# Kernel optimization log

Measured on AMD Instinct MI355X. Metric: run time of the kernel, lower is better.

The kernel has to match this reference:

```python
import jax, jax.numpy as jnp
import numpy as np
import math

EMBED_DIM = 512
NUM_HEADS = 8
NUM_EXPERTS = 16
TOP_K = 8
B, T = 2, 1024


def setup_inputs() -> dict:
    key = jax.random.key(0)
    ks = jax.random.split(key, 16)
    d, E = EMBED_DIM, NUM_EXPERTS
    hdim = 4 * d  # expert hidden width
    s = 0.02
    inp = {
        "x": jax.random.normal(ks[0], (B, T, d), jnp.float32),
        # RMSNorm params (init ones, matching torch module)
        "g": jnp.ones((d,), jnp.float32),
        "b": jnp.ones((d,), jnp.float32),
        # attention
        "c_attn_w": jax.random.normal(ks[1], (d, 3 * d), jnp.float32) * s,
        "c_attn_b": jnp.zeros((3 * d,), jnp.float32),
        "alpha": jnp.ones((NUM_HEADS,), jnp.float32),
        "c_proj_w": jax.random.normal(ks[2], (d, d), jnp.float32) * s,
        "c_proj_b": jnp.zeros((d,), jnp.float32),
        # router
        "router_w": jax.random.normal(ks[3], (d, E), jnp.float32) * s,
        "router_b": jnp.zeros((E,), jnp.float32),
        # stacked expert params: Linear(d,4d) -> SwiGLU(4d,4d) -> Linear(4d,d)
        "w_in": jax.random.normal(ks[4], (E, d, hdim), jnp.float32) * s,
        "b_in": jnp.zeros((E, hdim), jnp.float32),
        "w1": jax.random.normal(ks[5], (E, hdim, 2 * hdim), jnp.float32) * s,
        "b1": jnp.zeros((E, 2 * hdim), jnp.float32),
        "w2": jax.random.normal(ks[6], (E, hdim, hdim), jnp.float32) * s,
        "b2": jnp.zeros((E, hdim), jnp.float32),
        "w_out": jax.random.normal(ks[7], (E, hdim, d), jnp.float32) * s,
        "b_out": jnp.zeros((E, d), jnp.float32),
    }
    return inp


def _block(x, g, b, c_attn_w, c_attn_b, alpha, c_proj_w, c_proj_b,
           router_w, router_b, w_in, b_in, w1, b1, w2, b2, w_out, b_out):
    Bb, Tt, C = x.shape
    H = alpha.shape[0]
    hd = C // H
    E = router_b.shape[0]

    # RMSNorm (note: additive b, per original module)
    rms = jnp.sqrt(jnp.mean(x * x, axis=-1, keepdims=True) + 1e-6)
    xn = (x / rms) * g + b

    # QK-normalized causal attention
    qkv = xn @ c_attn_w + c_attn_b                      # [B,T,3C]
    q, k, v = jnp.split(qkv, 3, axis=-1)
    def heads(t):
        return t.reshape(Bb, Tt, H, hd).transpose(0, 2, 1, 3)  # [B,H,T,hd]
    q, k, v = heads(q), heads(k), heads(v)
    eps = 1e-5
    q_hat = q / (jnp.linalg.norm(q, axis=-1, keepdims=True) + eps)
    k_hat = k / (jnp.linalg.norm(k, axis=-1, keepdims=True) + eps)
    factor = (alpha * math.sqrt(hd)).reshape(1, H, 1, 1)
    q_scaled = q_hat * factor
    # SDPA default scale = 1/sqrt(head_dim)
    scores = jnp.einsum("bhqd,bhkd->bhqk", q_scaled, k_hat) / math.sqrt(hd)
    causal = jnp.tril(jnp.ones((Tt, Tt), bool))
    scores = jnp.where(causal, scores, -jnp.inf)
    att = jax.nn.softmax(scores, axis=-1)
    y = jnp.einsum("bhqk,bhkd->bhqd", att, v)
    y = y.transpose(0, 2, 1, 3).reshape(Bb, Tt, C)
    y = y @ c_proj_w + c_proj_b
    x = x + y

    # Router + top-8 normalized gates
    routes = jax.nn.softmax(x @ router_w + router_b, axis=-1)  # [B,T,E]
    probs, idx = jax.lax.top_k(routes, TOP_K)
    probs = probs / jnp.sum(probs, axis=-1, keepdims=True)
    # combine weights per expert: [B,T,E]
    gates = jnp.sum(jax.nn.one_hot(idx, E, dtype=x.dtype) * probs[..., None], axis=2)

    # Dense expert evaluation (faithful math: unselected tokens get zero gate)
    N = Bb * Tt
    xf = x.reshape(N, C)
    gf = gates.reshape(N, E)
    h = jnp.einsum("nd,edf->enf", xf, w_in) + b_in[:, None, :]      # [E,N,4d]
    c = jnp.einsum("enf,efg->eng", h, w1) + b1[:, None, :]          # [E,N,8d]
    a, bb2 = jnp.split(c, 2, axis=-1)
    s = (bb2 * jax.nn.sigmoid(bb2)) * a                              # SwiGLU
    o = jnp.einsum("enf,efg->eng", s, w2) + b2[:, None, :]          # [E,N,4d]
    eo = jnp.einsum("enf,efd->end", o, w_out) + b_out[:, None, :]   # [E,N,d]
    moe = jnp.einsum("end,ne->nd", eo, gf).reshape(Bb, Tt, C)
    return x + moe


def reference(x, g, b, c_attn_w, c_attn_b, alpha, c_proj_w, c_proj_b,
              router_w, router_b, w_in, b_in, w1, b1, w2, b2, w_out, b_out):
    return _block(x, g, b, c_attn_w, c_attn_b, alpha, c_proj_w, c_proj_b,
                  router_w, router_b, w_in, b_in, w1, b1, w2, b2, w_out, b_out)
```

## Files before the change

kernel.cpp:

```cpp
#include <hip/hip_runtime.h>
#include <stdint.h>

#define DEVI __device__ __forceinline__
#define FENCE() asm volatile("" ::: "memory")
#define BAR() do{ FENCE(); __builtin_amdgcn_s_barrier(); FENCE(); }while(0)

typedef short short8 __attribute__((ext_vector_type(8)));
typedef short short4v __attribute__((ext_vector_type(4)));
typedef float f32x4 __attribute__((ext_vector_type(4)));

DEVI float bf2f(unsigned short s){ union{unsigned u; float f;} x; x.u = ((unsigned)s)<<16; return x.f; }
DEVI unsigned short f2bf(float f){ union{float f; unsigned u;} x; x.f=f; unsigned r = x.u + 0x7fff + ((x.u>>16)&1); return (unsigned short)(r>>16); }

DEVI void gload_lds16(const void* g, void* l){
  __builtin_amdgcn_global_load_lds((const __attribute__((address_space(1))) unsigned int*)g,
                                   (__attribute__((address_space(3))) unsigned int*)l, 16, 0, 0);
}

__global__ __launch_bounds__(256)
void transpose_cvt(const float* __restrict__ in, unsigned short* __restrict__ out, int K, int N)
{
  __shared__ float tile[32][33];
  size_t zoff = (size_t)blockIdx.z * K * N;
  const float* src = in + zoff;
  unsigned short* dst = out + zoff;
  int kb = blockIdx.y*32, nb = blockIdx.x*32;
  int t = threadIdx.x;
  int tr = t>>3, tc = (t&7)*4;
  float4 v = *(const float4*)(src + (size_t)(kb+tr)*N + nb + tc);
  tile[tr][tc+0]=v.x; tile[tr][tc+1]=v.y; tile[tr][tc+2]=v.z; tile[tr][tc+3]=v.w;
  __syncthreads();
  short4v ov;
  ov[0] = (short)f2bf(tile[tc+0][tr]);
  ov[1] = (short)f2bf(tile[tc+1][tr]);
  ov[2] = (short)f2bf(tile[tc+2][tr]);
  ov[3] = (short)f2bf(tile[tc+3][tr]);
  *(short4v*)(dst + (size_t)(nb+tr)*K + kb + tc) = ov;
}

__global__ __launch_bounds__(256)
void rmsnorm_k(const float* __restrict__ x, const float* __restrict__ gw,
               const float* __restrict__ bw, unsigned short* __restrict__ xn)
{
  int row = blockIdx.x*4 + (threadIdx.x>>6);
  int lane = threadIdx.x & 63;
  const float* xr = x + (size_t)row*512 + lane*8;
  float4 a = *(const float4*)xr;
  float4 c = *(const float4*)(xr+4);
  float ss = a.x*a.x+a.y*a.y+a.z*a.z+a.w*a.w + c.x*c.x+c.y*c.y+c.z*c.z+c.w*c.w;
  #pragma unroll
  for (int m=1;m<64;m<<=1) ss += __shfl_xor(ss, m);
  float inv = 1.0f / sqrtf(ss*(1.f/512.f) + 1e-6f);
  const float* gr = gw + lane*8; const float* br = bw + lane*8;
  float4 g0=*(const float4*)gr, g1=*(const float4*)(gr+4);
  float4 b0=*(const float4*)br, b1=*(const float4*)(br+4);
  short8 o;
  o[0]=(short)f2bf(a.x*inv*g0.x + b0.x);
  o[1]=(short)f2bf(a.y*inv*g0.y + b0.y);
  o[2]=(short)f2bf(a.z*inv*g0.z + b0.z);
  o[3]=(short)f2bf(a.w*inv*g0.w + b0.w);
  o[4]=(short)f2bf(c.x*inv*g1.x + b1.x);
  o[5]=(short)f2bf(c.y*inv*g1.y + b1.y);
  o[6]=(short)f2bf(c.z*inv*g1.z + b1.z);
  o[7]=(short)f2bf(c.w*inv*g1.w + b1.w);
  *(short8*)(xn + (size_t)row*512 + lane*8) = o;
}

#define MFMA_QUAD(MQ) do{ \
  __builtin_amdgcn_s_setprio(1); \
  _Pragma("unroll") \
  for (int m=(MQ)*2; m<(MQ)*2+2; m++){ \
    _Pragma("unroll") \
    for (int n=0;n<4;n++){ \
      _Pragma("unroll") \
      for (int kk=0;kk<2;kk++) \
        acc[m][n] = __builtin_amdgcn_mfma_f32_16x16x32_bf16(afr[m][kk], bfr[n][kk], acc[m][n], 0,0,0); \
    } \
  } \
  __builtin_amdgcn_s_setprio(0); \
}while(0)

template<int EPI>
__global__ __launch_bounds__(512, 2)
void gemm8(const unsigned short* __restrict__ A, const unsigned short* __restrict__ B,
           const float* __restrict__ bias,
           float* __restrict__ Cf, unsigned short* __restrict__ Ch,
           const unsigned short* __restrict__ aux,
           int M, int N, int K,
           const int* __restrict__ off, long long strideBz, long long strideBiasz)
{
  __shared__ char smem[131072];
  int z = blockIdx.z;
  int rowbase = 0, Mz = M;
  if (off){ rowbase = off[z]; Mz = off[z+1] - rowbase; }
  int row0 = blockIdx.y * 256;
  if (row0 >= Mz) return;
  int col0 = blockIdx.x * 256;
  const unsigned short* Ab = A + (size_t)(rowbase + row0) * K;
  const unsigned short* Bb = B + (size_t)z * strideBz + (size_t)col0 * K;
  const float* biasz = bias + (size_t)z * strideBiasz;

  int tid = threadIdx.x;
  int lane = tid & 63, w = tid >> 6;
  int lrow = lane & 15, lg = lane >> 4;
  int wm = w >> 2, wn = w & 3;

  f32x4 acc[8][4];
  #pragma unroll
  for (int i=0;i<8;i++){
    #pragma unroll
    for (int j=0;j<4;j++) acc[i][j] = f32x4{0.f,0.f,0.f,0.f};
  }

  int nkt = K >> 6;

  auto stage = [&](int kt2, int H){
    if (kt2 >= nkt) return;
    char* sl = smem + (size_t)(kt2 & 1) * 65536 + (size_t)H * 16384;
    int k0 = kt2 << 6;
    const unsigned short* src = (H < 2) ? Ab : Bb;
    int rbase = (H & 1) * 128;
    #pragma unroll
    for (int i=0;i<2;i++){
      int si = i*512 + tid;
      int r = si >> 3, kb = (si & 7) ^ (r & 7);
      gload_lds16(src + (size_t)(rbase + r)*K + k0 + kb*8, sl + si*16);
    }
  };

  stage(0,0); stage(0,1); stage(0,2); stage(0,3);
  stage(1,0); stage(1,1); stage(1,2);
  asm volatile("s_waitcnt vmcnt(6)" ::: "memory");
  BAR();

  for (int kt = 0; kt < nkt; kt++){
    char* sl = smem + (size_t)(kt & 1) * 65536;
    char* sB = sl + 32768;
    short8 afr[8][2], bfr[4][2];
    #pragma unroll
    for (int n=0;n<4;n++){
      int ct = wn*64 + n*16 + lrow;
      #pragma unroll
      for (int kk=0;kk<2;kk++)
        bfr[n][kk] = *(const short8*)(sB + ct*128 + (((lg + kk*4) ^ (ct&7))<<4));
    }
    #pragma unroll
    for (int m=0;m<8;m++){
      int rt = wm*128 + m*16 + lrow;
      #pragma unroll
      for (int kk=0;kk<2;kk++)
        afr[m][kk] = *(const short8*)(sl + rt*128 + (((lg + kk*4) ^ (rt&7))<<4));
    }
    stage(kt+1, 3);
    BAR();
    asm volatile("s_waitcnt lgkmcnt(0)" ::: "memory");
    __builtin_amdgcn_sched_barrier(0);
    MFMA_QUAD(0);
    BAR();
    stage(kt+2, 0);
    BAR();
    MFMA_QUAD(1);
    BAR();
    stage(kt+2, 1);
    BAR();
    MFMA_QUAD(2);
    BAR();
    stage(kt+2, 2);
    if (kt + 2 < nkt) { asm volatile("s_waitcnt vmcnt(6)" ::: "memory"); }
    else              { asm volatile("s_waitcnt vmcnt(0)" ::: "memory"); }
    BAR();
    MFMA_QUAD(3);
    BAR();
  }

  #pragma unroll
  for (int m=0;m<8;m++){
    int rloc = wm*128 + m*16 + lg*4;
    #pragma unroll
    for (int j=0;j<4;j++){
      int row = row0 + rloc + j;
      if (row < Mz){
        size_t rg = (size_t)(rowbase + row);
        #pragma unroll
        for (int n=0;n<4;n++){
          int col = col0 + wn*64 + n*16 + lrow;
          float v = acc[m][n][j] + biasz[col];
          size_t idx = rg * N + col;
          if constexpr (EPI == 0){
            Cf[idx] = v;
          } else if constexpr (EPI == 1){
            Ch[idx] = f2bf(v);
          } else {
            float a = bf2f(aux[idx]);
            float sg = v / (1.f + __expf(-v));
            Ch[idx] = f2bf(a * sg);
          }
        }
      }
    }
  }
}

__global__ __launch_bounds__(256)
void gemm_proj(const unsigned short* __restrict__ A, const unsigned short* __restrict__ B,
               const float* __restrict__ bias,
               float* __restrict__ Cf, unsigned short* __restrict__ Ch,
               const float* __restrict__ resid, int M, int N, int K)
{
  __shared__ char smem[32768];
  char* smA = smem; char* smB = smem + 16384;
  int row0 = blockIdx.y * 128;
  int col0 = blockIdx.x * 128;
  int t = threadIdx.x, w = t>>6, lane = t&63;
  int lrow = lane&15, lg = lane>>4;
  int wr = w>>1, wc = w&1;

  f32x4 acc[4][4];
  #pragma unroll
  for (int i=0;i<4;i++){
    #pragma unroll
    for (int j=0;j<4;j++) acc[i][j] = f32x4{0.f,0.f,0.f,0.f};
  }
  const size_t Abase = (size_t)row0 * K;
  const size_t Bbase = (size_t)col0 * K;
  int nkt = K >> 6;
  for (int kt=0; kt<nkt; kt++){
    __syncthreads();
    int k0 = kt*64;
    #pragma unroll
    for (int i=0;i<4;i++){
      int s = (i*4 + w)*64 + lane;
      int r = s>>3;
      int kb = (s&7) ^ (r&7);
      gload_lds16(A + Abase + (size_t)r*K + k0 + kb*8, smA + (size_t)(i*4+w)*1024);
      gload_lds16(B + Bbase + (size_t)r*K + k0 + kb*8, smB + (size_t)(i*4+w)*1024);
    }
    __syncthreads();
    #pragma unroll
    for (int ks=0; ks<2; ks++){
      short8 af[4], bf[4];
      int kbb = lg + ks*4;
      #pragma unroll
      for (int m=0;m<4;m++){
        int rt = wr*64 + m*16 + lrow;
        af[m] = *(const short8*)(smA + rt*128 + ((kbb ^ (rt&7))<<4));
      }
      #pragma unroll
      for (int n=0;n<4;n++){
        int rt = wc*64 + n*16 + lrow;
        bf[n] = *(const short8*)(smB + rt*128 + ((kbb ^ (rt&7))<<4));
      }
      #pragma unroll
      for (int m=0;m<4;m++){
        #pragma unroll
        for (int n=0;n<4;n++)
          acc[m][n] = __builtin_amdgcn_mfma_f32_16x16x32_bf16(af[m], bf[n], acc[m][n], 0,0,0);
      }
    }
  }
  #pragma unroll
  for (int m=0;m<4;m++){
    int rloc = wr*64 + m*16 + lg*4;
    #pragma unroll
    for (int j=0;j<4;j++){
      int row = row0 + rloc + j;
      size_t rg = (size_t)row;
      #pragma unroll
      for (int n=0;n<4;n++){
        int col = col0 + wc*64 + n*16 + lrow;
        float v = acc[m][n][j] + bias[col];
        size_t idx = rg * N + col;
        v += resid[idx];
        Cf[idx] = v;
        Ch[idx] = f2bf(v);
      }
    }
  }
}

__global__ __launch_bounds__(256)
void prep_qkv(const float* __restrict__ qkv, const float* __restrict__ alpha,
              unsigned short* __restrict__ q_s, unsigned short* __restrict__ k_hat,
              unsigned short* __restrict__ v_t)
{
  int idx = blockIdx.x*4 + (threadIdx.x>>6);
  int lane = threadIdx.x & 63;
  int h = idx & 7, bt = idx >> 3;
  size_t base = (size_t)bt*1536 + h*64 + lane;
  float qv = qkv[base], kv = qkv[base+512], vv = qkv[base+1024];
  float qs2 = qv*qv, ks2 = kv*kv;
  #pragma unroll
  for (int m=1;m<64;m<<=1){ qs2 += __shfl_xor(qs2, m); ks2 += __shfl_xor(ks2, m); }
  float qh = qv / (sqrtf(qs2) + 1e-5f) * alpha[h];
  float kh = kv / (sqrtf(ks2) + 1e-5f);
  int b = bt >> 10, tt = bt & 1023;
  size_t hb = ((size_t)(b*8+h))*1024*64;
  q_s[hb + (size_t)tt*64 + lane] = f2bf(qh);
  k_hat[hb + (size_t)tt*64 + lane] = f2bf(kh);
  v_t[((size_t)(b*8+h)*64 + lane)*1024 + tt] = f2bf(vv);
}

__global__ __launch_bounds__(256)
void attn_k(const unsigned short* __restrict__ q_s, const unsigned short* __restrict__ k_hat,
            const unsigned short* __restrict__ v_t, unsigned short* __restrict__ y)
{
  __shared__ char sm[51200];
  char* smK = sm + 18432;
  char* smV = sm + 34816;
  int qt = blockIdx.x, bh = blockIdx.y;
  int b = bh>>3, h = bh&7;
  int t = threadIdx.x, w = t>>6, lane = t&63;
  int lrow = lane&15, lg = lane>>4;
  int q0 = qt*128;
  const size_t hQK = (size_t)bh*1024*64;
  const size_t hV  = (size_t)bh*64*1024;

  #pragma unroll
  for (int i=0;i<4;i++){
    int s = (i*4+w)*64 + lane;
    int r = s>>3, kb = (s&7)^(r&7);
    gload_lds16(q_s + hQK + (size_t)(q0+r)*64 + kb*8, sm + (size_t)(i*4+w)*1024);
  }
  __syncthreads();
  short8 qf[2][2];
  #pragma unroll
  for (int mf=0;mf<2;mf++){
    #pragma unroll
    for (int ks=0;ks<2;ks++){
      int rt = w*32 + mf*16 + lrow;
      int kbb = lg + ks*4;
      qf[mf][ks] = *(const short8*)(sm + rt*128 + ((kbb^(rt&7))<<4));
    }
  }
  f32x4 oacc[2][4];
  #pragma unroll
  for (int i=0;i<2;i++){
    #pragma unroll
    for (int j=0;j<4;j++) oacc[i][j] = f32x4{0.f,0.f,0.f,0.f};
  }
  float mrun[2][4], lrun[2][4];
  #pragma unroll
  for (int i=0;i<2;i++){
    #pragma unroll
    for (int j=0;j<4;j++){ mrun[i][j] = -1e30f; lrun[i][j] = 0.f; }
  }
  char* Pw = sm + w*4608;

  for (int kt=0; kt<=qt; kt++){
    __syncthreads();
    int t0 = kt*128;
    #pragma unroll
    for (int i=0;i<4;i++){
      int s = (i*4+w)*64 + lane;
      int r = s>>3, kb = (s&7)^(r&7);
      gload_lds16(k_hat + hQK + (size_t)(t0+r)*64 + kb*8, smK + (size_t)(i*4+w)*1024);
    }
    #pragma unroll
    for (int i=0;i<4;i++){
      int s = (i*4+w)*64 + lane;
      int d = s>>4, kb2 = s&15;
      int kb = kb2 ^ (d&7);
      gload_lds16(v_t + hV + (size_t)d*1024 + t0 + kb*8, smV + (size_t)(i*4+w)*1024);
    }
    __syncthreads();

    f32x4 sacc[2][8];
    #pragma unroll
    for (int i=0;i<2;i++){
      #pragma unroll
      for (int j=0;j<8;j++) sacc[i][j] = f32x4{0.f,0.f,0.f,0.f};
    }
    #pragma unroll
    for (int ks=0;ks<2;ks++){
      short8 kf[8];
      int kbb = lg + ks*4;
      #pragma unroll
      for (int nf=0;nf<8;nf++){
        int rt = nf*16+lrow;
        kf[nf] = *(const short8*)(smK + rt*128 + ((kbb^(rt&7))<<4));
      }
      #pragma unroll
      for (int mf=0;mf<2;mf++){
        #pragma unroll
        for (int nf=0;nf<8;nf++)
          sacc[mf][nf] = __builtin_amdgcn_mfma_f32_16x16x32_bf16(qf[mf][ks], kf[nf], sacc[mf][nf], 0,0,0);
      }
    }
    if (kt == qt){
      #pragma unroll
      for (int mf=0;mf<2;mf++){
        #pragma unroll
        for (int nf=0;nf<8;nf++){
          #pragma unroll
          for (int j=0;j<4;j++){
            int qi = w*32+mf*16+lg*4+j;
            int ki = nf*16 + lrow;
            if (ki > qi) sacc[mf][nf][j] = -1e30f;
          }
        }
      }
    }
    #pragma unroll
    for (int mf=0;mf<2;mf++){
      #pragma unroll
      for (int j=0;j<4;j++){
        float mx = sacc[mf][0][j];
        #pragma unroll
        for (int nf=1;nf<8;nf++) mx = fmaxf(mx, sacc[mf][nf][j]);
        #pragma unroll
        for (int m=1;m<16;m<<=1) mx = fmaxf(mx, __shfl_xor(mx, m));
        float mnew = fmaxf(mrun[mf][j], mx);
        float sc = __expf(mrun[mf][j] - mnew);
        float rs = 0.f;
        #pragma unroll
        for (int nf=0;nf<8;nf++){
          float p = __expf(sacc[mf][nf][j] - mnew);
          sacc[mf][nf][j] = p; rs += p;
        }
        #pragma unroll
        for (int m=1;m<16;m<<=1) rs += __shfl_xor(rs, m);
        lrun[mf][j] = lrun[mf][j]*sc + rs;
        mrun[mf][j] = mnew;
        #pragma unroll
        for (int n2=0;n2<4;n2++) oacc[mf][n2][j] *= sc;
      }
    }
    #pragma unroll
    for (int half=0; half<2; half++){
      #pragma unroll
      for (int mf=0;mf<2;mf++){
        #pragma unroll
        for (int nfh=0;nfh<4;nfh++){
          int nf = half*4 + nfh;
          #pragma unroll
          for (int j=0;j<4;j++){
            int row = mf*16 + lg*4 + j;
            int col = nfh*16 + lrow;
            *(unsigned short*)(Pw + (row*72 + col)*2) = f2bf(sacc[mf][nf][j]);
          }
        }
      }
      #pragma unroll
      for (int k2=0;k2<2;k2++){
        int ks2 = half*2 + k2;
        short8 pf[2], vf[4];
        #pragma unroll
        for (int mf=0;mf<2;mf++)
          pf[mf] = *(const short8*)(Pw + (mf*16+lrow)*144 + lg*16 + k2*64);
        #pragma unroll
        for (int n2=0;n2<4;n2++){
          int d = n2*16+lrow;
          int kbb2 = lg + ks2*4;
          vf[n2] = *(const short8*)(smV + d*256 + ((kbb2^(d&7))<<4));
        }
        #pragma unroll
        for (int mf=0;mf<2;mf++){
          #pragma unroll
          for (int n2=0;n2<4;n2++)
            oacc[mf][n2] = __builtin_amdgcn_mfma_f32_16x16x32_bf16(pf[mf], vf[n2], oacc[mf][n2], 0,0,0);
        }
      }
    }
  }
  #pragma unroll
  for (int mf=0;mf<2;mf++){
    #pragma unroll
    for (int n2=0;n2<4;n2++){
      #pragma unroll
      for (int j=0;j<4;j++){
        float v = oacc[mf][n2][j] / lrun[mf][j];
        int qi = q0 + w*32 + mf*16 + lg*4 + j;
        int d = n2*16 + lrow;
        y[((size_t)(b*1024+qi))*512 + h*64 + d] = f2bf(v);
      }
    }
  }
}

__global__ __launch_bounds__(256)
void router_topk(const float* __restrict__ x2f, const float* __restrict__ rw,
                 const float* __restrict__ rb, float* __restrict__ gates)
{
  int tkn = blockIdx.x*4 + (threadIdx.x>>6);
  int lane = threadIdx.x & 63;
  int e = lane & 15, p = lane >> 4;
  const float* xr = x2f + (size_t)tkn*512;
  float part = 0.f;
  for (int d = p*128; d < p*128+128; d++)
    part += xr[d] * rw[d*16 + e];
  part += __shfl_xor(part, 16);
  part += __shfl_xor(part, 32);
  float logit = part + rb[e];
  float mx = logit;
  #pragma unroll
  for (int m=1;m<16;m<<=1) mx = fmaxf(mx, __shfl_xor(mx, m));
  float ex = __expf(logit - mx);
  float sm = ex;
  #pragma unroll
  for (int m=1;m<16;m<<=1) sm += __shfl_xor(sm, m);
  float prob = ex / sm;
  bool taken = false;
  float ssum = 0.f;
  #pragma unroll
  for (int r=0;r<8;r++){
    float cv = taken ? -1.f : prob;
    int ci = e;
    #pragma unroll
    for (int m=1;m<16;m<<=1){
      float ov = __shfl_xor(cv, m);
      int oi = __shfl_xor(ci, m);
      if (ov > cv || (ov == cv && oi < ci)){ cv = ov; ci = oi; }
    }
    if (e == ci) taken = true;
    ssum += cv;
  }
  if (lane < 16)
    gates[(size_t)tkn*16 + e] = taken ? prob / ssum : 0.f;
}

__global__ void listbuild(const float* __restrict__ gates, int* __restrict__ list,
                          int* __restrict__ slot, int* __restrict__ cnt)
{
  int e = blockIdx.x;
  int tid = threadIdx.x, w = tid>>6, lane = tid&63;
  __shared__ int sbase;
  __shared__ int wsum[4];
  if (tid==0) sbase = 0;
  __syncthreads();
  for (int c=0;c<8;c++){
    int tk = c*256 + tid;
    bool flag = gates[(size_t)tk*16 + e] > 0.f;
    unsigned long long bal = __ballot(flag);
    if (lane==0) wsum[w] = (int)__popcll(bal);
    __syncthreads();
    int wpref = 0;
    for (int i=0;i<w;i++) wpref += wsum[i];
    int tot = wsum[0]+wsum[1]+wsum[2]+wsum[3];
    int lpref = (int)__popcll(bal & ((1ull<<lane)-1ull));
    if (flag){
      int pos = sbase + wpref + lpref;
      list[e*2048 + pos] = tk;
      slot[(size_t)tk*16 + e] = pos;
    }
    __syncthreads();
    if (tid==0) sbase += tot;
    __syncthreads();
  }
  if (tid==0) cnt[e] = sbase;
}

__global__ void prefix_off(const int* __restrict__ cnt, int* __restrict__ off){
  if (threadIdx.x==0 && blockIdx.x==0){
    int a=0;
    for (int e=0;e<16;e++){ off[e]=a; a+=cnt[e]; }
    off[16]=a;
  }
}

__global__ __launch_bounds__(256)
void gather_rows(const unsigned short* __restrict__ x2h, const int* __restrict__ list,
                 const int* __restrict__ cnt, const int* __restrict__ off,
                 unsigned short* __restrict__ xe)
{
  int e = blockIdx.y;
  int s = blockIdx.x*4 + (threadIdx.x>>6);
  if (s >= cnt[e]) return;
  int lane = threadIdx.x & 63;
  int tk = list[e*2048 + s];
  *(short8*)(xe + ((size_t)(off[e]+s))*512 + lane*8) =
      *(const short8*)(x2h + (size_t)tk*512 + lane*8);
}

__global__ __launch_bounds__(256)
void combine_k(const float* __restrict__ x2f, const unsigned short* __restrict__ eo,
               const float* __restrict__ gates, const int* __restrict__ slot,
               const int* __restrict__ off, float* __restrict__ out)
{
  int tkn = blockIdx.x;
  __shared__ float gs[16];
  __shared__ int rws[16];
  int tid = threadIdx.x;
  if (tid < 16){
    float g = gates[(size_t)tkn*16 + tid];
    gs[tid] = g;
    rws[tid] = (g > 0.f) ? (off[tid] + slot[(size_t)tkn*16 + tid]) : 0;
  }
  __syncthreads();
  for (int d = tid; d < 512; d += 256){
    float v = x2f[(size_t)tkn*512 + d];
    #pragma unroll
    for (int e=0;e<16;e++){
      float g = gs[e];
      if (g > 0.f) v += g * bf2f(eo[(size_t)rws[e]*512 + d]);
    }
    out[(size_t)tkn*512 + d] = v;
  }
}

extern "C" void kernel_launch(void* const* d_in, const int* in_sizes, int n_in,
                              void* d_out, int out_size, void* d_ws, size_t ws_size,
                              hipStream_t stream) {
  (void)in_sizes; (void)n_in; (void)out_size; (void)ws_size;
  const float* x    = (const float*)d_in[0];
  const float* gw   = (const float*)d_in[1];
  const float* bw   = (const float*)d_in[2];
  const float* caw  = (const float*)d_in[3];
  const float* cab  = (const float*)d_in[4];
  const float* alpha= (const float*)d_in[5];
  const float* cpw  = (const float*)d_in[6];
  const float* cpb  = (const float*)d_in[7];
  const float* rw   = (const float*)d_in[8];
  const float* rb   = (const float*)d_in[9];
  const float* w_in = (const float*)d_in[10];
  const float* b_in = (const float*)d_in[11];
  const float* w1   = (const float*)d_in[12];
  const float* b1   = (const float*)d_in[13];
  const float* w2   = (const float*)d_in[14];
  const float* b2   = (const float*)d_in[15];
  const float* w_out= (const float*)d_in[16];
  const float* b_out= (const float*)d_in[17];

  char* ws = (char*)d_ws;
  size_t o = 0;
  auto alloc = [&](size_t bytes)->char*{
    char* p = ws + o;
    o += (bytes + 255) & ~(size_t)255;
    return p;
  };
  const size_t PADROWS = 16896;
  unsigned short* wT_attn = (unsigned short*)alloc(1536ull*512*2);
  unsigned short* wT_proj = (unsigned short*)alloc(512ull*512*2);
  unsigned short* wT_in   = (unsigned short*)alloc(16ull*2048*512*2);
  unsigned short* wT_1    = (unsigned short*)alloc(16ull*4096*2048*2);
  unsigned short* wT_2    = (unsigned short*)alloc(16ull*2048*2048*2);
  unsigned short* wT_out  = (unsigned short*)alloc(16ull*512*2048*2);
  unsigned short* xn      = (unsigned short*)alloc(2048ull*512*2);
  float*          qkv     = (float*)alloc(2048ull*1536*4);
  unsigned short* q_s     = (unsigned short*)alloc(2048ull*512*2);
  unsigned short* k_hat   = (unsigned short*)alloc(2048ull*512*2);
  unsigned short* v_t     = (unsigned short*)alloc(2048ull*512*2);
  unsigned short* ybuf    = (unsigned short*)alloc(2048ull*512*2);
  float*          x2f     = (float*)alloc(2048ull*512*4);
  unsigned short* x2h     = (unsigned short*)alloc(2048ull*512*2);
  float*          gates   = (float*)alloc(2048ull*16*4);
  int*            slot    = (int*)alloc(2048ull*16*4);
  int*            list    = (int*)alloc(16ull*2048*4);
  int*            cnt     = (int*)alloc(64);
  int*            off     = (int*)alloc(256);
  unsigned short* xe      = (unsigned short*)alloc(PADROWS*512*2);
  unsigned short* hbuf    = (unsigned short*)alloc(PADROWS*2048*2);
  unsigned short* c1buf   = (unsigned short*)alloc(PADROWS*2048*2);
  unsigned short* sbuf    = (unsigned short*)alloc(PADROWS*2048*2);
  unsigned short* eobuf   = xe;
  unsigned short* obuf    = hbuf;

  dim3 blk(256);
  dim3 blk5(512);
  transpose_cvt<<<dim3(1536/32, 512/32, 1), blk, 0, stream>>>(caw, wT_attn, 512, 1536);
  transpose_cvt<<<dim3(512/32, 512/32, 1), blk, 0, stream>>>(cpw, wT_proj, 512, 512);
  transpose_cvt<<<dim3(2048/32, 512/32, 16), blk, 0, stream>>>(w_in, wT_in, 512, 2048);
  transpose_cvt<<<dim3(4096/32, 2048/32, 16), blk, 0, stream>>>(w1, wT_1, 2048, 4096);
  transpose_cvt<<<dim3(2048/32, 2048/32, 16), blk, 0, stream>>>(w2, wT_2, 2048, 2048);
  transpose_cvt<<<dim3(512/32, 2048/32, 16), blk, 0, stream>>>(w_out, wT_out, 2048, 512);

  rmsnorm_k<<<512, blk, 0, stream>>>(x, gw, bw, xn);
  gemm8<0><<<dim3(6, 8, 1), blk5, 0, stream>>>(xn, wT_attn, cab, qkv, nullptr, nullptr,
                                               2048, 1536, 512, nullptr, 0, 0);
  prep_qkv<<<4096, blk, 0, stream>>>(qkv, alpha, q_s, k_hat, v_t);
  attn_k<<<dim3(8,16), blk, 0, stream>>>(q_s, k_hat, v_t, ybuf);
  gemm_proj<<<dim3(4,16,1), blk, 0, stream>>>(ybuf, wT_proj, cpb, x2f, x2h, x, 2048, 512, 512);
  router_topk<<<512, blk, 0, stream>>>(x2f, rw, rb, gates);
  listbuild<<<16, blk, 0, stream>>>(gates, list, slot, cnt);
  prefix_off<<<1, 64, 0, stream>>>(cnt, off);
  gather_rows<<<dim3(512,16), blk, 0, stream>>>(x2h, list, cnt, off, xe);

  gemm8<1><<<dim3(8,8,16), blk5, 0, stream>>>(xe, wT_in, b_in, nullptr, hbuf, nullptr,
                                              0, 2048, 512, off, 2048ll*512, 2048);
  gemm8<1><<<dim3(8,8,16), blk5, 0, stream>>>(hbuf, wT_1, b1, nullptr, c1buf, nullptr,
                                              0, 2048, 2048, off, 4096ll*2048, 4096);
  gemm8<2><<<dim3(8,8,16), blk5, 0, stream>>>(hbuf, wT_1 + 2048ull*2048, b1 + 2048, nullptr, sbuf,
                                              c1buf, 0, 2048, 2048, off, 4096ll*2048, 4096);
  gemm8<1><<<dim3(8,8,16), blk5, 0, stream>>>(sbuf, wT_2, b2, nullptr, obuf, nullptr,
                                              0, 2048, 2048, off, 2048ll*2048, 2048);
  gemm8<1><<<dim3(2,8,16), blk5, 0, stream>>>(obuf, wT_out, b_out, nullptr, eobuf, nullptr,
                                              0, 512, 2048, off, 512ll*2048, 512);
  combine_k<<<2048, blk, 0, stream>>>(x2f, eobuf, gates, slot, off, (float*)d_out);
}
```

Before: 1.221 ms.

## Fuse MoE expert pipeline into persistent kernel with grid barriers and interleaved SwiGLU

Replaces the gather, five grouped GEMM launches and the combine kernel with one persistent 256-block kernel that runs each stage and separates stages with atomic grid-wide barriers. Expert row segments are padded to multiples of 128 so tiles never straddle experts. The w1 weight is transposed with gate and up columns interleaved per 16-column group, so one GEMM computes both halves and applies SwiGLU in its epilogue, removing the c1buf round trip. Tiles shrink to 128x256 and the LDS pipeline is reworked. The grid barriers rely on all 256 blocks being co-resident, and the padding adds wasted rows.

Measured after the change: 1.835 ms. 50.3% more time.

```diff
diff --git a/kernel.cpp b/kernel.cpp
--- a/kernel.cpp
+++ b/kernel.cpp
@@ -39,6 +39,30 @@
 }
 
 __global__ __launch_bounds__(256)
+void transpose_cvt_w1(const float* __restrict__ w1, unsigned short* __restrict__ outp)
+{
+  __shared__ float tile[32][33];
+  int e = blockIdx.z;
+  const float* src = w1 + (size_t)e*2048*4096;
+  unsigned short* dst = outp + (size_t)e*4096*2048;
+  int np0 = blockIdx.x*32;
+  int k0 = blockIdx.y*32;
+  int g = np0 >> 5;
+  int t = threadIdx.x;
+  int tr = t>>3, tc = (t&7)*4;
+  int srccol = (tc < 16) ? (g*16 + tc) : (2048 + g*16 + (tc-16));
+  float4 v = *(const float4*)(src + (size_t)(k0+tr)*4096 + srccol);
+  tile[tr][tc+0]=v.x; tile[tr][tc+1]=v.y; tile[tr][tc+2]=v.z; tile[tr][tc+3]=v.w;
+  __syncthreads();
+  short4v ov;
+  ov[0] = (short)f2bf(tile[tc+0][tr]);
+  ov[1] = (short)f2bf(tile[tc+1][tr]);
+  ov[2] = (short)f2bf(tile[tc+2][tr]);
+  ov[3] = (short)f2bf(tile[tc+3][tr]);
+  *(short4v*)(dst + (size_t)(np0+tr)*2048 + k0 + tc) = ov;
+}
+
+__global__ __launch_bounds__(256)
 void rmsnorm_k(const float* __restrict__ x, const float* __restrict__ gw,
                const float* __restrict__ bw, unsigned short* __restrict__ xn)
 {
@@ -80,25 +104,16 @@
   __builtin_amdgcn_s_setprio(0); \
 }while(0)
 
-template<int EPI>
 __global__ __launch_bounds__(512, 2)
-void gemm8(const unsigned short* __restrict__ A, const unsigned short* __restrict__ B,
-           const float* __restrict__ bias,
-           float* __restrict__ Cf, unsigned short* __restrict__ Ch,
-           const unsigned short* __restrict__ aux,
-           int M, int N, int K,
-           const int* __restrict__ off, long long strideBz, long long strideBiasz)
+void gemm8_f32(const unsigned short* __restrict__ A, const unsigned short* __restrict__ B,
+               const float* __restrict__ bias, float* __restrict__ Cf,
+               int M, int N, int K)
 {
   __shared__ char smem[131072];
-  int z = blockIdx.z;
-  int rowbase = 0, Mz = M;
-  if (off){ rowbase = off[z]; Mz = off[z+1] - rowbase; }
   int row0 = blockIdx.y * 256;
-  if (row0 >= Mz) return;
   int col0 = blockIdx.x * 256;
-  const unsigned short* Ab = A + (size_t)(rowbase + row0) * K;
-  const unsigned short* Bb = B + (size_t)z * strideBz + (size_t)col0 * K;
-  const float* biasz = bias + (size_t)z * strideBiasz;
+  const unsigned short* Ab = A + (size_t)row0 * K;
+  const unsigned short* Bb = B + (size_t)col0 * K;
 
   int tid = threadIdx.x;
   int lane = tid & 63, w = tid >> 6;
@@ -111,9 +126,7 @@
     #pragma unroll
     for (int j=0;j<4;j++) acc[i][j] = f32x4{0.f,0.f,0.f,0.f};
   }
-
   int nkt = K >> 6;
-
   auto stage = [&](int kt2, int H){
     if (kt2 >= nkt) return;
     char* sl = smem + (size_t)(kt2 & 1) * 65536 + (size_t)H * 16384;
@@ -127,12 +140,10 @@
       gload_lds16(src + (size_t)(rbase + r)*K + k0 + kb*8, sl + si*16);
     }
   };
-
   stage(0,0); stage(0,1); stage(0,2); stage(0,3);
   stage(1,0); stage(1,1); stage(1,2);
   asm volatile("s_waitcnt vmcnt(6)" ::: "memory");
   BAR();
-
   for (int kt = 0; kt < nkt; kt++){
     char* sl = smem + (size_t)(kt & 1) * 65536;
     char* sB = sl + 32768;
@@ -172,30 +183,16 @@
     MFMA_QUAD(3);
     BAR();
   }
-
   #pragma unroll
   for (int m=0;m<8;m++){
     int rloc = wm*128 + m*16 + lg*4;
     #pragma unroll
     for (int j=0;j<4;j++){
       int row = row0 + rloc + j;
-      if (row < Mz){
-        size_t rg = (size_t)(rowbase + row);
-        #pragma unroll
-        for (int n=0;n<4;n++){
-          int col = col0 + wn*64 + n*16 + lrow;
-          float v = acc[m][n][j] + biasz[col];
-          size_t idx = rg * N + col;
-          if constexpr (EPI == 0){
-            Cf[idx] = v;
-          } else if constexpr (EPI == 1){
-            Ch[idx] = f2bf(v);
-          } else {
-            float a = bf2f(aux[idx]);
-            float sg = v / (1.f + __expf(-v));
-            Ch[idx] = f2bf(a * sg);
-          }
-        }
+      #pragma unroll
+      for (int n=0;n<4;n++){
+        int col = col0 + wn*64 + n*16 + lrow;
+        Cf[(size_t)row * N + col] = acc[m][n][j] + bias[col];
       }
     }
   }
@@ -549,51 +546,238 @@
   if (tid==0) cnt[e] = sbase;
 }
 
-__global__ void prefix_off(const int* __restrict__ cnt, int* __restrict__ off){
+__global__ void prefix_off(const int* __restrict__ cnt, int* __restrict__ off,
+                           int* __restrict__ bars){
   if (threadIdx.x==0 && blockIdx.x==0){
     int a=0;
-    for (int e=0;e<16;e++){ off[e]=a; a+=cnt[e]; }
+    for (int e=0;e<16;e++){ off[e]=a; a += (cnt[e]+127)&~127; }
     off[16]=a;
-  }
-}
-
-__global__ __launch_bounds__(256)
-void gather_rows(const unsigned short* __restrict__ x2h, const int* __restrict__ list,
-                 const int* __restrict__ cnt, const int* __restrict__ off,
-                 unsigned short* __restrict__ xe)
-{
-  int e = blockIdx.y;
-  int s = blockIdx.x*4 + (threadIdx.x>>6);
-  if (s >= cnt[e]) return;
-  int lane = threadIdx.x & 63;
-  int tk = list[e*2048 + s];
-  *(short8*)(xe + ((size_t)(off[e]+s))*512 + lane*8) =
-      *(const short8*)(x2h + (size_t)tk*512 + lane*8);
-}
-
-__global__ __launch_bounds__(256)
-void combine_k(const float* __restrict__ x2f, const unsigned short* __restrict__ eo,
-               const float* __restrict__ gates, const int* __restrict__ slot,
-               const int* __restrict__ off, float* __restrict__ out)
-{
-  int tkn = blockIdx.x;
-  __shared__ float gs[16];
-  __shared__ int rws[16];
-  int tid = threadIdx.x;
-  if (tid < 16){
-    float g = gates[(size_t)tkn*16 + tid];
-    gs[tid] = g;
-    rws[tid] = (g > 0.f) ? (off[tid] + slot[(size_t)tkn*16 + tid]) : 0;
-  }
+    for (int i=0;i<8;i++) bars[i]=0;
+  }
+}
+
+DEVI void gsync(int* bar){
   __syncthreads();
-  for (int d = tid; d < 512; d += 256){
-    float v = x2f[(size_t)tkn*512 + d];
-    #pragma unroll
+  if (threadIdx.x == 0){
+    __threadfence();
+    __hip_atomic_fetch_add(bar, 1, __ATOMIC_ACQ_REL, __HIP_MEMORY_SCOPE_AGENT);
+    while (__hip_atomic_load(bar, __ATOMIC_ACQUIRE, __HIP_MEMORY_SCOPE_AGENT) < 256)
+      __builtin_amdgcn_s_sleep(8);
+  }
+  __syncthreads();
+  __threadfence();
+}
+
+template<int EPI>
+DEVI void mega_tile(const unsigned short* __restrict__ Ab,
+                    const unsigned short* __restrict__ Bb,
+                    const float* __restrict__ bias,
+                    unsigned short* __restrict__ outp,
+                    int N, int K, int outRowBase, int col0,
+                    char* smem, int tid)
+{
+  int lane = tid & 63, w = tid >> 6;
+  int lrow = lane & 15, lg = lane >> 4;
+  int wm = w >> 2, wn = w & 3;
+  f32x4 acc[4][4];
+  #pragma unroll
+  for (int i=0;i<4;i++){
+    #pragma unroll
+    for (int j=0;j<4;j++) acc[i][j] = f32x4{0.f,0.f,0.f,0.f};
+  }
+  int nkt = K >> 6;
+  auto stage = [&](int kt2, int U){
+    if (kt2 >= nkt) return;
+    char* sl = smem + (kt2 & 1) * 49152 + U * 16384;
+    int k0 = kt2 << 6;
+    const unsigned short* src = (U == 0) ? Ab : Bb;
+    int rbase = (U == 0) ? 0 : (U-1)*128;
+    #pragma unroll
+    for (int i=0;i<2;i++){
+      int si = i*512 + tid;
+      int r = si >> 3, kb = (si & 7) ^ (r & 7);
+      gload_lds16(src + (size_t)(rbase + r)*K + k0 + kb*8, sl + si*16);
+    }
+  };
+  stage(0,0); stage(0,1); stage(0,2); stage(1,0); stage(1,1);
+  asm volatile("s_waitcnt vmcnt(4)" ::: "memory");
+  BAR();
+  for (int kt=0; kt<nkt; kt++){
+    char* sA = smem + (kt&1)*49152;
+    char* sB = sA + 16384;
+    short8 afr[4][2], bfr[4][2];
+    #pragma unroll
+    for (int n=0;n<4;n++){
+      int ct = wn*64 + n*16 + lrow;
+      #pragma unroll
+      for (int kk=0;kk<2;kk++)
+        bfr[n][kk] = *(const short8*)(sB + ct*128 + (((lg+kk*4) ^ (ct&7))<<4));
+    }
+    #pragma unroll
+    for (int m=0;m<4;m++){
+      int rt = wm*64 + m*16 + lrow;
+      #pragma unroll
+      for (int kk=0;kk<2;kk++)
+        afr[m][kk] = *(const short8*)(sA + rt*128 + (((lg+kk*4) ^ (rt&7))<<4));
+    }
+    stage(kt+1, 2);
+    BAR();
+    asm volatile("s_waitcnt lgkmcnt(0)" ::: "memory");
+    __builtin_amdgcn_sched_barrier(0);
+    __builtin_amdgcn_s_setprio(1);
+    #pragma unroll
+    for (int m=0;m<4;m++){
+      #pragma unroll
+      for (int n=0;n<4;n++)
+        acc[m][n] = __builtin_amdgcn_mfma_f32_16x16x32_bf16(afr[m][0], bfr[n][0], acc[m][n], 0,0,0);
+    }
+    __builtin_amdgcn_s_setprio(0);
+    BAR();
+    stage(kt+2, 0);
+    stage(kt+2, 1);
+    if (kt+2 < nkt) { asm volatile("s_waitcnt vmcnt(4)" ::: "memory"); }
+    else            { asm volatile("s_waitcnt vmcnt(0)" ::: "memory"); }
+    BAR();
+    __builtin_amdgcn_s_setprio(1);
+    #pragma unroll
+    for (int m=0;m<4;m++){
+      #pragma unroll
+      for (int n=0;n<4;n++)
+        acc[m][n] = __builtin_amdgcn_mfma_f32_16x16x32_bf16(afr[m][1], bfr[n][1], acc[m][n], 0,0,0);
+    }
+    __builtin_amdgcn_s_setprio(0);
+    BAR();
+  }
+  if constexpr (EPI == 1){
+    #pragma unroll
+    for (int m=0;m<4;m++){
+      #pragma unroll
+      for (int j=0;j<4;j++){
+        int row = outRowBase + wm*64 + m*16 + lg*4 + j;
+        #pragma unroll
+        for (int n=0;n<4;n++){
+          int col = col0 + wn*64 + n*16 + lrow;
+          outp[(size_t)row*N + col] = f2bf(acc[m][n][j] + bias[col]);
+        }
+      }
+    }
+  } else {
+    #pragma unroll
+    for (int m=0;m<4;m++){
+      #pragma unroll
+      for (int j=0;j<4;j++){
+        int row = outRowBase + wm*64 + m*16 + lg*4 + j;
+        #pragma unroll
+        for (int nf=0;nf<4;nf+=2){
+          int pcol = col0 + wn*64 + nf*16;
+          int scol = ((pcol>>5)<<4) + lrow;
+          float av = acc[m][nf][j]   + bias[scol];
+          float gv = acc[m][nf+1][j] + bias[2048 + scol];
+          float sg = gv / (1.f + __expf(-gv));
+          outp[(size_t)row*2048 + scol] = f2bf(av * sg);
+        }
+      }
+    }
+  }
+}
+
+__global__ __launch_bounds__(512, 2)
+void moe_mega(const unsigned short* __restrict__ x2h,
+              const int* __restrict__ list, const int* __restrict__ cnt,
+              const int* __restrict__ off, const float* __restrict__ gates,
+              const int* __restrict__ slot, const float* __restrict__ x2f,
+              const unsigned short* __restrict__ wT_in, const float* __restrict__ b_in,
+              const unsigned short* __restrict__ wT1p, const float* __restrict__ b1,
+              const unsigned short* __restrict__ wT_2, const float* __restrict__ b2,
+              const unsigned short* __restrict__ wT_out, const float* __restrict__ b_out,
+              unsigned short* __restrict__ xe, unsigned short* __restrict__ hbuf,
+              unsigned short* __restrict__ sbuf, unsigned short* __restrict__ obuf,
+              unsigned short* __restrict__ eobuf, float* __restrict__ out,
+              int* __restrict__ bars)
+{
+  __shared__ char smem[98304];
+  __shared__ int soff[17];
+  int tid = threadIdx.x, bid = blockIdx.x;
+  if (tid < 17) soff[tid] = off[tid];
+  __syncthreads();
+  int rowsp = soff[16];
+  int RT = rowsp >> 7;
+
+  for (int r0 = bid*8; r0 < rowsp; r0 += 2048){
+    int r = r0 + (tid>>6);
+    if (r < rowsp){
+      int e = 0;
+      while (e < 15 && soff[e+1] <= r) e++;
+      int s = r - soff[e];
+      int lane8 = (tid&63)*8;
+      short8 v = short8{0,0,0,0,0,0,0,0};
+      if (s < cnt[e]){
+        int tk = list[e*2048 + s];
+        v = *(const short8*)(x2h + (size_t)tk*512 + lane8);
+      }
+      *(short8*)(xe + (size_t)r*512 + lane8) = v;
+    }
+  }
+  gsync(bars+0);
+
+  for (int t = bid; t < RT*8; t += 256){
+    int rt = t >> 3, ct = t & 7;
+    int row = rt << 7;
+    int e = 0; while (e < 15 && soff[e+1] <= row) e++;
+    mega_tile<1>(xe + (size_t)row*512,
+                 wT_in + (size_t)e*2048*512 + (size_t)(ct*256)*512,
+                 b_in + e*2048, hbuf, 2048, 512, row, ct*256, smem, tid);
+  }
+  gsync(bars+1);
+
+  for (int t = bid; t < RT*16; t += 256){
+    int rt = t >> 4, ct = t & 15;
+    int row = rt << 7;
+    int e = 0; while (e < 15 && soff[e+1] <= row) e++;
+    mega_tile<2>(hbuf + (size_t)row*2048,
+                 wT1p + (size_t)e*4096*2048 + (size_t)(ct*256)*2048,
+                 b1 + e*4096, sbuf, 4096, 2048, row, ct*256, smem, tid);
+  }
+  gsync(bars+2);
+
+  for (int t = bid; t < RT*8; t += 256){
+    int rt = t >> 3, ct = t & 7;
+    int row = rt << 7;
+    int e = 0; while (e < 15 && soff[e+1] <= row) e++;
+    mega_tile<1>(sbuf + (size_t)row*2048,
+                 wT_2 + (size_t)e*2048*2048 + (size_t)(ct*256)*2048,
+                 b2 + e*2048, obuf, 2048, 2048, row, ct*256, smem, tid);
+  }
+  gsync(bars+3);
+
+  for (int t = bid; t < RT*2; t += 256){
+    int rt = t >> 1, ct = t & 1;
+    int row = rt << 7;
+    int e = 0; while (e < 15 && soff[e+1] <= row) e++;
+    mega_tile<1>(obuf + (size_t)row*2048,
+                 wT_out + (size_t)e*512*2048 + (size_t)(ct*256)*2048,
+                 b_out + e*512, eobuf, 512, 2048, row, ct*256, smem, tid);
+  }
+  gsync(bars+4);
+
+  {
+    int tkn = bid*8 + (tid>>6);
+    int lane8 = (tid&63)*8;
+    float v[8];
+    const float* xr = x2f + (size_t)tkn*512 + lane8;
+    #pragma unroll
+    for (int i=0;i<8;i++) v[i] = xr[i];
     for (int e=0;e<16;e++){
-      float g = gs[e];
-      if (g > 0.f) v += g * bf2f(eo[(size_t)rws[e]*512 + d]);
-    }
-    out[(size_t)tkn*512 + d] = v;
+      float g = gates[(size_t)tkn*16 + e];
+      if (g > 0.f){
+        int rw = soff[e] + slot[(size_t)tkn*16 + e];
+        short8 ev = *(const short8*)(eobuf + (size_t)rw*512 + lane8);
+        #pragma unroll
+        for (int i=0;i<8;i++) v[i] += g * bf2f((unsigned short)ev[i]);
+      }
+    }
+    #pragma unroll
+    for (int i=0;i<8;i++) out[(size_t)tkn*512 + lane8 + i] = v[i];
   }
 }
 
@@ -627,11 +811,11 @@
     o += (bytes + 255) & ~(size_t)255;
     return p;
   };
-  const size_t PADROWS = 16896;
+  const size_t PADROWS = 18432;
   unsigned short* wT_attn = (unsigned short*)alloc(1536ull*512*2);
   unsigned short* wT_proj = (unsigned short*)alloc(512ull*512*2);
   unsigned short* wT_in   = (unsigned short*)alloc(16ull*2048*512*2);
-  unsigned short* wT_1    = (unsigned short*)alloc(16ull*4096*2048*2);
+  unsigned short* wT1p    = (unsigned short*)alloc(16ull*4096*2048*2);
   unsigned short* wT_2    = (unsigned short*)alloc(16ull*2048*2048*2);
   unsigned short* wT_out  = (unsigned short*)alloc(16ull*512*2048*2);
   unsigned short* xn      = (unsigned short*)alloc(2048ull*512*2);
@@ -647,9 +831,9 @@
   int*            list    = (int*)alloc(16ull*2048*4);
   int*            cnt     = (int*)alloc(64);
   int*            off     = (int*)alloc(256);
+  int*            bars    = (int*)alloc(64);
   unsigned short* xe      = (unsigned short*)alloc(PADROWS*512*2);
   unsigned short* hbuf    = (unsigned short*)alloc(PADROWS*2048*2);
-  unsigned short* c1buf   = (unsigned short*)alloc(PADROWS*2048*2);
   unsigned short* sbuf    = (unsigned short*)alloc(PADROWS*2048*2);
   unsigned short* eobuf   = xe;
   unsigned short* obuf    = hbuf;
@@ -659,30 +843,20 @@
   transpose_cvt<<<dim3(1536/32, 512/32, 1), blk, 0, stream>>>(caw, wT_attn, 512, 1536);
   transpose_cvt<<<dim3(512/32, 512/32, 1), blk, 0, stream>>>(cpw, wT_proj, 512, 512);
   transpose_cvt<<<dim3(2048/32, 512/32, 16), blk, 0, stream>>>(w_in, wT_in, 512, 2048);
-  transpose_cvt<<<dim3(4096/32, 2048/32, 16), blk, 0, stream>>>(w1, wT_1, 2048, 4096);
+  transpose_cvt_w1<<<dim3(4096/32, 2048/32, 16), blk, 0, stream>>>(w1, wT1p);
   transpose_cvt<<<dim3(2048/32, 2048/32, 16), blk, 0, stream>>>(w2, wT_2, 2048, 2048);
   transpose_cvt<<<dim3(512/32, 2048/32, 16), blk, 0, stream>>>(w_out, wT_out, 2048, 512);
 
   rmsnorm_k<<<512, blk, 0, stream>>>(x, gw, bw, xn);
-  gemm8<0><<<dim3(6, 8, 1), blk5, 0, stream>>>(xn, wT_attn, cab, qkv, nullptr, nullptr,
-                                               2048, 1536, 512, nullptr, 0, 0);
+  gemm8_f32<<<dim3(6, 8, 1), blk5, 0, stream>>>(xn, wT_attn, cab, qkv, 2048, 1536, 512);
   prep_qkv<<<4096, blk, 0, stream>>>(qkv, alpha, q_s, k_hat, v_t);
   attn_k<<<dim3(8,16), blk, 0, stream>>>(q_s, k_hat, v_t, ybuf);
   gemm_proj<<<dim3(4,16,1), blk, 0, stream>>>(ybuf, wT_proj, cpb, x2f, x2h, x, 2048, 512, 512);
   router_topk<<<512, blk, 0, stream>>>(x2f, rw, rb, gates);
   listbuild<<<16, blk, 0, stream>>>(gates, list, slot, cnt);
-  prefix_off<<<1, 64, 0, stream>>>(cnt, off);
-  gather_rows<<<dim3(512,16), blk, 0, stream>>>(x2h, list, cnt, off, xe);
-
-  gemm8<1><<<dim3(8,8,16), blk5, 0, stream>>>(xe, wT_in, b_in, nullptr, hbuf, nullptr,
-                                              0, 2048, 512, off, 2048ll*512, 2048);
-  gemm8<1><<<dim3(8,8,16), blk5, 0, stream>>>(hbuf, wT_1, b1, nullptr, c1buf, nullptr,
-                                              0, 2048, 2048, off, 4096ll*2048, 4096);
-  gemm8<2><<<dim3(8,8,16), blk5, 0, stream>>>(hbuf, wT_1 + 2048ull*2048, b1 + 2048, nullptr, sbuf,
-                                              c1buf, 0, 2048, 2048, off, 4096ll*2048, 4096);
-  gemm8<1><<<dim3(8,8,16), blk5, 0, stream>>>(sbuf, wT_2, b2, nullptr, obuf, nullptr,
-                                              0, 2048, 2048, off, 2048ll*2048, 2048);
-  gemm8<1><<<dim3(2,8,16), blk5, 0, stream>>>(obuf, wT_out, b_out, nullptr, eobuf, nullptr,
-                                              0, 512, 2048, off, 512ll*2048, 512);
-  combine_k<<<2048, blk, 0, stream>>>(x2f, eobuf, gates, slot, off, (float*)d_out);
-}
+  prefix_off<<<1, 64, 0, stream>>>(cnt, off, bars);
+
+  moe_mega<<<256, blk5, 0, stream>>>(x2h, list, cnt, off, gates, slot, x2f,
+                                     wT_in, b_in, wT1p, b1, wT_2, b2, wT_out, b_out,
+                                     xe, hbuf, sbuf, obuf, eobuf, (float*)d_out, bars);
+}
```
